# Performance work log

Hardware: AMD Instinct MI355X
Metric: run time of the kernel (lower is better)

## Reference

```python
import jax, jax.numpy as jnp
import numpy as np
from jax import lax

B, CIN, HW = 4, 3, 256      # batch, image channels, image size
HID = 128                   # hidden_size
EMB_D = 64                  # embedding_dim == encoder output channels
K = 1024                    # num_embeddings
L = 2                       # num encoder/decoder layers (1 resblock each)


def _conv(x, w, b, stride, pad):
    y = lax.conv_general_dilated(x, w, (stride, stride), ((pad, pad), (pad, pad)),
                                 dimension_numbers=('NCHW', 'OIHW', 'NCHW'))
    return y + b[None, :, None, None]


def _bn(x):
    # BatchNorm2d in training mode: batch stats over (N,H,W), affine at init (gamma=1, beta=0)
    m = x.mean((0, 2, 3), keepdims=True)
    v = x.var((0, 2, 3), keepdims=True)
    return (x - m) * lax.rsqrt(v + 1e-5)


def _resblock(x, w1, b1, w2, b2):
    y = jax.nn.relu(_bn(_conv(x, w1, b1, 1, 1)))
    y = _bn(_conv(y, w2, b2, 1, 1))
    return jax.nn.relu(y + x)


def _conv_t(x, w, b):
    # torch ConvTranspose2d(k=4, s=2, p=1); w in torch layout (I, O, 4, 4)
    wf = jnp.flip(w, (2, 3)).transpose(1, 0, 2, 3)  # (O, I, 4, 4)
    y = lax.conv_general_dilated(x, wf, (1, 1), ((2, 2), (2, 2)), lhs_dilation=(2, 2),
                                 dimension_numbers=('NCHW', 'OIHW', 'NCHW'))
    return y + b[None, :, None, None]


def _vqvae(x, enc_in_w, enc_in_b, enc_res_w1, enc_res_b1, enc_res_w2, enc_res_b2,
           enc_down_w, enc_down_b, enc_out_w, enc_out_b,
           dec_in_w, dec_in_b, dec_res_w1, dec_res_b1, dec_res_w2, dec_res_b2,
           dec_up_w, dec_up_b, dec_out_w, dec_out_b, codebook):
    sg = lax.stop_gradient
    # ---- encoder ----
    h = _conv(x, enc_in_w, enc_in_b, 1, 0)
    for i in range(L):
        h = _resblock(h, enc_res_w1[i], enc_res_b1[i], enc_res_w2[i], enc_res_b2[i])
        h = jax.nn.relu(_conv(h, enc_down_w[i], enc_down_b[i], 2, 1))
    z = _conv(h, enc_out_w, enc_out_b, 1, 0)  # (B, C, H/4, W/4)
    # ---- vector quantize ----
    Bz, C, Hl, Wl = z.shape
    zf = z.transpose(0, 2, 3, 1).reshape(-1, C)  # (N, C)
    # ||z - e||^2 expanded; same argmin as the (N,K,C) form without materializing it
    d = (zf * zf).sum(1, keepdims=True) - 2.0 * (zf @ codebook.T) + (codebook * codebook).sum(1)[None, :]
    idx = jnp.argmin(d, axis=1)  # (N,)
    z_q = codebook[idx].reshape(Bz, Hl, Wl, C).transpose(0, 3, 1, 2)
    z_q_st = z_q + sg(z - z_q)  # as in source: forward value == z, grads flow to codebook
    # ---- decoder ----
    h = _conv(z_q_st, dec_in_w, dec_in_b, 1, 0)
    for i in range(L):
        h = _resblock(h, dec_res_w1[i], dec_res_b1[i], dec_res_w2[i], dec_res_b2[i])
        h = jax.nn.relu(_conv_t(h, dec_up_w[i], dec_up_b[i]))
    recon = jax.nn.sigmoid(_conv(h, dec_out_w, dec_out_b, 1, 0))
    # ---- losses ----
    commit = jnp.mean((z - sg(z_q_st)) ** 2)
    cb_l = jnp.mean((sg(z) - z_q_st) ** 2)
    counts = jnp.zeros((K,), jnp.float32).at[idx].add(1.0)
    p = counts + 1e-6
    p = p / p.sum()
    ent = -(p * jnp.log(p)).sum()
    loss = commit + cb_l - ent
    return recon, loss, idx.reshape(Bz, Hl, Wl)


def setup_inputs() -> dict:
    key = jax.random.key(0)
    ks = iter(jax.random.split(key, 40))
    def w(shape, fan_in):
        return jax.random.normal(next(ks), shape, jnp.float32) * np.float32((2.0 / fan_in) ** 0.5)
    z128 = lambda *s: jnp.zeros(s, jnp.float32)
    return {
        'x': jax.random.uniform(next(ks), (B, CIN, HW, HW), jnp.float32),
        'enc_in_w': w((HID, CIN, 1, 1), CIN), 'enc_in_b': z128(HID),
        'enc_res_w1': w((L, HID, HID, 3, 3), HID * 9), 'enc_res_b1': z128(L, HID),
        'enc_res_w2': w((L, HID, HID, 3, 3), HID * 9), 'enc_res_b2': z128(L, HID),
        'enc_down_w': w((L, HID, HID, 4, 4), HID * 16), 'enc_down_b': z128(L, HID),
        'enc_out_w': w((EMB_D, HID, 1, 1), HID), 'enc_out_b': z128(EMB_D),
        'dec_in_w': w((HID, EMB_D, 1, 1), EMB_D), 'dec_in_b': z128(HID),
        'dec_res_w1': w((L, HID, HID, 3, 3), HID * 9), 'dec_res_b1': z128(L, HID),
        'dec_res_w2': w((L, HID, HID, 3, 3), HID * 9), 'dec_res_b2': z128(L, HID),
        'dec_up_w': w((L, HID, HID, 4, 4), HID * 16), 'dec_up_b': z128(L, HID),  # (I,O,4,4) torch layout
        'dec_out_w': w((CIN, HID, 1, 1), HID), 'dec_out_b': z128(CIN),
        'codebook': jax.random.normal(next(ks), (K, EMB_D), jnp.float32) * np.float32((2.0 / (K + EMB_D)) ** 0.5),
    }


def reference(x, enc_in_w, enc_in_b, enc_res_w1, enc_res_b1, enc_res_w2, enc_res_b2,
              enc_down_w, enc_down_b, enc_out_w, enc_out_b,
              dec_in_w, dec_in_b, dec_res_w1, dec_res_b1, dec_res_w2, dec_res_b2,
              dec_up_w, dec_up_b, dec_out_w, dec_out_b, codebook):
    return _vqvae(x, enc_in_w, enc_in_b, enc_res_w1, enc_res_b1, enc_res_w2, enc_res_b2,
                  enc_down_w, enc_down_b, enc_out_w, enc_out_b,
                  dec_in_w, dec_in_b, dec_res_w1, dec_res_b1, dec_res_w2, dec_res_b2,
                  dec_up_w, dec_up_b, dec_out_w, dec_out_b, codebook)
```

## Files before the change

kernel.cpp:

```cpp
#include <hip/hip_runtime.h>
#include <math.h>


#define RE_SIZE 786432

typedef float f32x4 __attribute__((ext_vector_type(4)));
typedef short bf16x8 __attribute__((ext_vector_type(8)));
typedef short bf16x4 __attribute__((ext_vector_type(4)));

__device__ __forceinline__ unsigned short f2bf(float f) {
  unsigned u = __float_as_uint(f);
  return (unsigned short)((u + 0x7fffu + ((u >> 16) & 1u)) >> 16);
}
__device__ __forceinline__ float bf2f(unsigned short h) {
  return __uint_as_float(((unsigned)h) << 16);
}
__device__ __forceinline__ void split3(float v, unsigned short& a,
                                       unsigned short& b, unsigned short& c) {
  a = f2bf(v); float r = v - bf2f(a);
  b = f2bf(r); r -= bf2f(b);
  c = f2bf(r);
}

__global__ __launch_bounds__(256) void weff_kernel(
    const float* __restrict__ w3, const float* __restrict__ ew,
    const float* __restrict__ eb, unsigned short* __restrict__ f0,
    unsigned short* __restrict__ f1, unsigned short* __restrict__ f2) {
  int id = blockIdx.x * 256 + threadIdx.x;
  int j = id & 7, lane = (id >> 3) & 63, mt = (id >> 9) & 7, kc = id >> 12;
  int co = mt * 16 + (lane & 15);
  int q = lane >> 4;
  int k = kc * 32 + q * 8 + j;
  int t = k >> 2, c = k & 3;
  float v = 0.f;
  if (t <= 8) {
    double acc = 0.0;
    for (int ci = 0; ci < 128; ++ci) {
      double wv = (double)w3[((long)co * 128 + ci) * 9 + t];
      double xv = (c < 3) ? (double)ew[ci * 3 + c] : (double)eb[ci];
      acc += wv * xv;
    }
    v = (float)acc;
  }
  unsigned short a, b, cc; split3(v, a, b, cc);
  f0[id] = a; f1[id] = b; f2[id] = cc;
}

__global__ __launch_bounds__(256) void conv36_mfma_kernel(
    const float* __restrict__ xin, const unsigned short* __restrict__ f0,
    const unsigned short* __restrict__ f1, const unsigned short* __restrict__ f2,
    const float* __restrict__ bias, float* __restrict__ out, int H, int W) {
  __shared__ __align__(16) unsigned short s_x[3][720];
  int tid = threadIdx.x, wv = tid >> 6, lane = tid & 63;
  int q = lane >> 4, c15 = lane & 15;
  int tilesX = W >> 4;
  int tx0 = (blockIdx.x % tilesX) << 4;
  int ty0 = (blockIdx.x / tilesX) << 3;
  int n = blockIdx.z;
  long HWl = (long)H * W;
  long ibase = (long)n * 128 * HWl;
  long xbase = (long)n * 3 * HWl;
  f32x4 acc[2][8];
#pragma unroll
  for (int a = 0; a < 2; ++a)
#pragma unroll
    for (int b = 0; b < 8; ++b) acc[a][b] = (f32x4){0.f, 0.f, 0.f, 0.f};

  for (int l = tid; l < 180; l += 256) {
    int y = l / 18, x = l % 18;
    int gy = ty0 + y - 1, gx = tx0 + x - 1;
    float v[4] = {0.f, 0.f, 0.f, 0.f};
    if ((unsigned)gy < (unsigned)H && (unsigned)gx < (unsigned)W) {
      const float* xp = xin + xbase + (long)gy * W + gx;
      v[0] = xp[0]; v[1] = xp[HWl]; v[2] = xp[2 * HWl]; v[3] = 1.f;
    }
    bf16x4 s0, s1, s2;
#pragma unroll
    for (int c = 0; c < 4; ++c) {
      unsigned short h0, h1, h2; split3(v[c], h0, h1, h2);
      s0[c] = (short)h0; s1[c] = (short)h1; s2[c] = (short)h2;
    }
    *(bf16x4*)(s_x[0] + l * 4) = s0;
    *(bf16x4*)(s_x[1] + l * 4) = s1;
    *(bf16x4*)(s_x[2] + l * 4) = s2;
  }
  __syncthreads();

#pragma unroll
  for (int kc = 0; kc < 2; ++kc) {
    bf16x8 a0[2], a1[2], a2[2];
#pragma unroll
    for (int m = 0; m < 2; ++m) {
      long fi = (long)(kc * 8 + 2 * wv + m) * 64 + lane;
      a0[m] = ((const bf16x8*)f0)[fi];
      a1[m] = ((const bf16x8*)f1)[fi];
      a2[m] = ((const bf16x8*)f2)[fi];
    }
    int ta = kc * 8 + 2 * q; if (ta > 8) ta = 8;
    int tb = ta + 1;         if (tb > 8) tb = 8;
    int pa_d = (ta / 3) * 18 + ta % 3;
    int pb_d = (tb / 3) * 18 + tb % 3;
#pragma unroll
    for (int nn = 0; nn < 8; ++nn) {
      int pa = (nn * 18 + c15 + pa_d) * 4;
      int pb = (nn * 18 + c15 + pb_d) * 4;
      bf16x8 b0, b1v, b2;
      bf16x4 lo, hi;
      lo = *(const bf16x4*)(s_x[0] + pa); hi = *(const bf16x4*)(s_x[0] + pb);
#pragma unroll
      for (int i = 0; i < 4; ++i) { b0[i] = lo[i]; b0[4 + i] = hi[i]; }
      lo = *(const bf16x4*)(s_x[1] + pa); hi = *(const bf16x4*)(s_x[1] + pb);
#pragma unroll
      for (int i = 0; i < 4; ++i) { b1v[i] = lo[i]; b1v[4 + i] = hi[i]; }
      lo = *(const bf16x4*)(s_x[2] + pa); hi = *(const bf16x4*)(s_x[2] + pb);
#pragma unroll
      for (int i = 0; i < 4; ++i) { b2[i] = lo[i]; b2[4 + i] = hi[i]; }
#pragma unroll
      for (int m = 0; m < 2; ++m) {
        acc[m][nn] = __builtin_amdgcn_mfma_f32_16x16x32_bf16(a0[m], b0, acc[m][nn], 0, 0, 0);
        acc[m][nn] = __builtin_amdgcn_mfma_f32_16x16x32_bf16(a0[m], b1v, acc[m][nn], 0, 0, 0);
        acc[m][nn] = __builtin_amdgcn_mfma_f32_16x16x32_bf16(a1[m], b0, acc[m][nn], 0, 0, 0);
        acc[m][nn] = __builtin_amdgcn_mfma_f32_16x16x32_bf16(a0[m], b2, acc[m][nn], 0, 0, 0);
        acc[m][nn] = __builtin_amdgcn_mfma_f32_16x16x32_bf16(a1[m], b1v, acc[m][nn], 0, 0, 0);
        acc[m][nn] = __builtin_amdgcn_mfma_f32_16x16x32_bf16(a2[m], b0, acc[m][nn], 0, 0, 0);
      }
    }
  }
#pragma unroll
  for (int mt2 = 0; mt2 < 2; ++mt2) {
    int co0 = (wv * 2 + mt2) * 16 + q * 4;
#pragma unroll
    for (int nn = 0; nn < 8; ++nn) {
      long pxoff = ibase + (long)(ty0 + nn) * W + tx0 + c15;
#pragma unroll
      for (int r = 0; r < 4; ++r)
        out[pxoff + (long)(co0 + r) * HWl] = acc[mt2][nn][r] + bias[co0 + r];
    }
  }
}

__global__ __launch_bounds__(256) void wsplit_kernel(
    const float* __restrict__ w, unsigned short* __restrict__ w0,
    unsigned short* __restrict__ w1, unsigned short* __restrict__ w2) {
  int id = blockIdx.x * 256 + threadIdx.x;
  int j = id & 7, lane = (id >> 3) & 63, rest = id >> 9;
  int mt = rest & 7, rest2 = rest >> 3;
  int tap = rest2 % 9, cc = rest2 / 9;
  int co = mt * 16 + (lane & 15);
  int ci = cc * 32 + (lane >> 4) * 8 + j;
  float v = w[((long)co * 128 + ci) * 9 + tap];
  unsigned short a, b, c; split3(v, a, b, c);
  w0[id] = a; w1[id] = b; w2[id] = c;
}

__global__ __launch_bounds__(256) void wsplit4_kernel(
    const float* __restrict__ w, unsigned short* __restrict__ w0,
    unsigned short* __restrict__ w1, unsigned short* __restrict__ w2) {
  int id = blockIdx.x * 256 + threadIdx.x;
  int j = id & 7, lane = (id >> 3) & 63;
  int mt = (id >> 9) & 7, pair = (id >> 12) & 7, cc = id >> 15;
  int q = lane >> 4;
  int tap = pair * 2 + (q >> 1);
  int ky = tap >> 2, kx = tap & 3;
  int co = mt * 16 + (lane & 15);
  int ci = cc * 16 + (q & 1) * 8 + j;
  float v = w[((long)co * 128 + ci) * 16 + ky * 4 + kx];
  unsigned short a, b, c; split3(v, a, b, c);
  w0[id] = a; w1[id] = b; w2[id] = c;
}

__global__ __launch_bounds__(256) void wsplitT_kernel(
    const float* __restrict__ w, unsigned short* __restrict__ w0,
    unsigned short* __restrict__ w1) {
  int id = blockIdx.x * 256 + threadIdx.x;
  int jj = id & 7, lane = (id >> 3) & 63;
  int mt = (id >> 9) & 7, j = (id >> 12) & 3, cls = (id >> 14) & 3, cc = id >> 16;
  int py = cls >> 1, px = cls & 1, jy = j >> 1, jx = j & 1;
  int ky = py ? (jy ? 2 : 0) : (jy ? 3 : 1);
  int kx = px ? (jx ? 2 : 0) : (jx ? 3 : 1);
  int co = mt * 16 + (lane & 15);
  int ci = cc * 32 + (lane >> 4) * 8 + jj;
  float v = w[((long)ci * 128 + co) * 16 + ky * 4 + kx];
  unsigned short h = f2bf(v);
  w0[id] = h;
  w1[id] = f2bf(v - bf2f(h));
}

template<int IMODE, int SPLIT>
__global__ __launch_bounds__(256) void conv3x3_mfma_kernel(
    const float* __restrict__ in, const unsigned short* __restrict__ w0s,
    const unsigned short* __restrict__ w1s, const unsigned short* __restrict__ w2s,
    const float* __restrict__ bias, float* __restrict__ out, int H, int W,
    const float2* __restrict__ mr, const float* __restrict__ xin,
    const float* __restrict__ w1, const float* __restrict__ b1) {
  __shared__ __align__(16) unsigned short s_x[SPLIT][5760];
  int tid = threadIdx.x, wv = tid >> 6, lane = tid & 63;
  int q = lane >> 4, c15 = lane & 15;
  int tilesX = W >> 4;
  int tx0 = (blockIdx.x % tilesX) << 4;
  int ty0 = (blockIdx.x / tilesX) << 3;
  int n = blockIdx.z;
  long HWl = (long)H * W;
  long ibase = (long)n * 128 * HWl;
  f32x4 acc[2][8];
#pragma unroll
  for (int a = 0; a < 2; ++a)
#pragma unroll
    for (int b = 0; b < 8; ++b) acc[a][b] = (f32x4){0.f, 0.f, 0.f, 0.f};

  for (int cc = 0; cc < 4; ++cc) {
    __syncthreads();
    for (int l = tid; l < 720; l += 256) {
      int cig = l / 180, px = l % 180;
      int y = px / 18, x = px % 18;
      int gy = ty0 + y - 1, gx = tx0 + x - 1;
      float v[8];
      if ((unsigned)gy < (unsigned)H && (unsigned)gx < (unsigned)W) {
        if (IMODE == 2) {
          const float* xp = xin + (long)n * 3 * HWl + (long)gy * W + gx;
          float x0 = xp[0], x1 = xp[HWl], x2 = xp[2 * HWl];
#pragma unroll
          for (int c = 0; c < 8; ++c) {
            int ci = cc * 32 + cig * 8 + c;
            v[c] = fmaf(w1[ci * 3 + 0], x0,
                   fmaf(w1[ci * 3 + 1], x1,
                   fmaf(w1[ci * 3 + 2], x2, b1[ci])));
          }
        } else {
          const float* ip = in + ibase + (long)(cc * 32 + cig * 8) * HWl
                            + (long)gy * W + gx;
#pragma unroll
          for (int c = 0; c < 8; ++c) v[c] = ip[(long)c * HWl];
          if (IMODE == 1) {
#pragma unroll
            for (int c = 0; c < 8; ++c) {
              float2 s = mr[cc * 32 + cig * 8 + c];
              v[c] = fmaxf((v[c] - s.x) * s.y, 0.f);
            }
          }
        }
      } else {
#pragma unroll
        for (int c = 0; c < 8; ++c) v[c] = 0.f;
      }
      bf16x8 sv[SPLIT];
#pragma unroll
      for (int c = 0; c < 8; ++c) {
        unsigned short h0 = f2bf(v[c]); float r = v[c] - bf2f(h0);
        unsigned short h1 = f2bf(r);
        sv[0][c] = (short)h0; sv[1][c] = (short)h1;
        if (SPLIT == 3) { r -= bf2f(h1); sv[2][c] = (short)f2bf(r); }
      }
#pragma unroll
      for (int s = 0; s < SPLIT; ++s) *(bf16x8*)(s_x[s] + l * 8) = sv[s];
    }
    __syncthreads();

    for (int tap = 0; tap < 9; ++tap) {
      int dy = tap / 3, dx = tap % 3;
      long fbase = (long)((cc * 9 + tap) * 8) * 64;
      bf16x8 a0[2], a1[2], a2[2];
#pragma unroll
      for (int m = 0; m < 2; ++m) {
        long fi = fbase + (2 * wv + m) * 64 + lane;
        a0[m] = ((const bf16x8*)w0s)[fi];
        a1[m] = ((const bf16x8*)w1s)[fi];
        if (SPLIT == 3) a2[m] = ((const bf16x8*)w2s)[fi];
      }
      int xoff = (q * 180 + dy * 18 + c15 + dx) * 8;
#pragma unroll
      for (int nn = 0; nn < 8; ++nn) {
        bf16x8 b0 = *(const bf16x8*)(s_x[0] + xoff + nn * 144);
        bf16x8 b1v = *(const bf16x8*)(s_x[1] + xoff + nn * 144);
#pragma unroll
        for (int m = 0; m < 2; ++m) {
          acc[m][nn] = __builtin_amdgcn_mfma_f32_16x16x32_bf16(a0[m], b0, acc[m][nn], 0, 0, 0);
          acc[m][nn] = __builtin_amdgcn_mfma_f32_16x16x32_bf16(a0[m], b1v, acc[m][nn], 0, 0, 0);
          acc[m][nn] = __builtin_amdgcn_mfma_f32_16x16x32_bf16(a1[m], b0, acc[m][nn], 0, 0, 0);
        }
        if (SPLIT == 3) {
          bf16x8 b2 = *(const bf16x8*)(s_x[2] + xoff + nn * 144);
#pragma unroll
          for (int m = 0; m < 2; ++m) {
            acc[m][nn] = __builtin_amdgcn_mfma_f32_16x16x32_bf16(a0[m], b2, acc[m][nn], 0, 0, 0);
            acc[m][nn] = __builtin_amdgcn_mfma_f32_16x16x32_bf16(a1[m], b1v, acc[m][nn], 0, 0, 0);
            acc[m][nn] = __builtin_amdgcn_mfma_f32_16x16x32_bf16(a2[m], b0, acc[m][nn], 0, 0, 0);
          }
        }
      }
    }
  }
#pragma unroll
  for (int mt2 = 0; mt2 < 2; ++mt2) {
    int co0 = (wv * 2 + mt2) * 16 + q * 4;
#pragma unroll
    for (int nn = 0; nn < 8; ++nn) {
      long pxoff = ibase + (long)(ty0 + nn) * W + tx0 + c15;
#pragma unroll
      for (int r = 0; r < 4; ++r)
        out[pxoff + (long)(co0 + r) * HWl] = acc[mt2][nn][r] + bias[co0 + r];
    }
  }
}

__global__ __launch_bounds__(256) void down_mfma_kernel(
    const float* __restrict__ in, const unsigned short* __restrict__ w0s,
    const unsigned short* __restrict__ w1s, const unsigned short* __restrict__ w2s,
    const float* __restrict__ bias, float* __restrict__ out, int Hin, int Win) {
  __shared__ __align__(16) unsigned short s_x[3][9792];
  int tid = threadIdx.x, wv = tid >> 6, lane = tid & 63;
  int q = lane >> 4, c15 = lane & 15;
  int Hout = Hin >> 1, Wout = Win >> 1;
  int tilesX = Wout >> 4;
  int tx0 = (blockIdx.x % tilesX) << 4;
  int ty0 = (blockIdx.x / tilesX) << 3;
  int n = blockIdx.z;
  long HWin = (long)Hin * Win, HWout = (long)Hout * Wout;
  long ibase = (long)n * 128 * HWin, obase = (long)n * 128 * HWout;
  f32x4 acc[2][8];
#pragma unroll
  for (int a = 0; a < 2; ++a)
#pragma unroll
    for (int b = 0; b < 8; ++b) acc[a][b] = (f32x4){0.f, 0.f, 0.f, 0.f};

  for (int cc = 0; cc < 8; ++cc) {
    __syncthreads();
    for (int l = tid; l < 1224; l += 256) {
      int cig = l / 612, rem = l % 612;
      int g = rem / 153, p = rem % 153;
      int py = p / 17, px_ = p % 17;
      int gy = g >> 1, gx = g & 1;
      int iy = 2 * (ty0 + py - gy) + gy;
      int ix = 2 * (tx0 + px_ - gx) + gx;
      float v[8];
      if ((unsigned)iy < (unsigned)Hin && (unsigned)ix < (unsigned)Win) {
        const float* ip = in + ibase + (long)(cc * 16 + cig * 8) * HWin
                          + (long)iy * Win + ix;
#pragma unroll
        for (int c = 0; c < 8; ++c) v[c] = ip[(long)c * HWin];
      } else {
#pragma unroll
        for (int c = 0; c < 8; ++c) v[c] = 0.f;
      }
      bf16x8 s0, s1, s2;
#pragma unroll
      for (int c = 0; c < 8; ++c) {
        unsigned short h0, h1, h2; split3(v[c], h0, h1, h2);
        s0[c] = (short)h0; s1[c] = (short)h1; s2[c] = (short)h2;
      }
      *(bf16x8*)(s_x[0] + l * 8) = s0;
      *(bf16x8*)(s_x[1] + l * 8) = s1;
      *(bf16x8*)(s_x[2] + l * 8) = s2;
    }
    __syncthreads();

    for (int pr = 0; pr < 8; ++pr) {
      long fbase = (long)((cc * 8 + pr) * 8) * 64;
      bf16x8 a0[2], a1[2], a2[2];
#pragma unroll
      for (int m = 0; m < 2; ++m) {
        long fi = fbase + (2 * wv + m) * 64 + lane;
        a0[m] = ((const bf16x8*)w0s)[fi];
        a1[m] = ((const bf16x8*)w1s)[fi];
        a2[m] = ((const bf16x8*)w2s)[fi];
      }
      int tap = pr * 2 + (q >> 1);
      int ky = tap >> 2, kx = tap & 3;
      int gy = (ky + 1) & 1, gx = (kx + 1) & 1;
      int dy = (ky == 0) ? -1 : ((ky == 3) ? 1 : 0);
      int dx = (kx == 0) ? -1 : ((kx == 3) ? 1 : 0);
      int g = gy * 2 + gx, cig = q & 1;
      int xoff = ((cig * 4 + g) * 153 + (dy + gy) * 17 + (c15 + dx + gx)) * 8;
#pragma unroll
      for (int nn = 0; nn < 8; ++nn) {
        bf16x8 b0 = *(const bf16x8*)(s_x[0] + xoff + nn * 136);
        bf16x8 b1v = *(const bf16x8*)(s_x[1] + xoff + nn * 136);
        bf16x8 b2 = *(const bf16x8*)(s_x[2] + xoff + nn * 136);
#pragma unroll
        for (int m = 0; m < 2; ++m) {
          acc[m][nn] = __builtin_amdgcn_mfma_f32_16x16x32_bf16(a0[m], b0, acc[m][nn], 0, 0, 0);
          acc[m][nn] = __builtin_amdgcn_mfma_f32_16x16x32_bf16(a0[m], b1v, acc[m][nn], 0, 0, 0);
          acc[m][nn] = __builtin_amdgcn_mfma_f32_16x16x32_bf16(a1[m], b0, acc[m][nn], 0, 0, 0);
          acc[m][nn] = __builtin_amdgcn_mfma_f32_16x16x32_bf16(a0[m], b2, acc[m][nn], 0, 0, 0);
          acc[m][nn] = __builtin_amdgcn_mfma_f32_16x16x32_bf16(a1[m], b1v, acc[m][nn], 0, 0, 0);
          acc[m][nn] = __builtin_amdgcn_mfma_f32_16x16x32_bf16(a2[m], b0, acc[m][nn], 0, 0, 0);
        }
      }
    }
  }
#pragma unroll
  for (int mt2 = 0; mt2 < 2; ++mt2) {
    int co0 = (wv * 2 + mt2) * 16 + q * 4;
#pragma unroll
    for (int nn = 0; nn < 8; ++nn) {
      long pxoff = obase + (long)(ty0 + nn) * Wout + tx0 + c15;
#pragma unroll
      for (int r = 0; r < 4; ++r)
        out[pxoff + (long)(co0 + r) * HWout] =
            fmaxf(acc[mt2][nn][r] + bias[co0 + r], 0.f);
    }
  }
}

__global__ __launch_bounds__(256) void up_mfma_kernel(
    const float* __restrict__ in, const unsigned short* __restrict__ wh,
    const unsigned short* __restrict__ wl, const float* __restrict__ bias,
    float* __restrict__ out, int Hin, int Win) {
  __shared__ __align__(16) unsigned short s_xh[5760];
  __shared__ __align__(16) unsigned short s_xl[5760];
  int tid = threadIdx.x, wv = tid >> 6, lane = tid & 63;
  int q = lane >> 4, c15 = lane & 15;
  int cls = blockIdx.z & 3, n = blockIdx.z >> 2;
  int py = cls >> 1, px = cls & 1;
  int Hout = Hin << 1, Wout = Win << 1;
  int tilesX = Win >> 4;
  int x0 = (blockIdx.x % tilesX) << 4;
  int m0 = (blockIdx.x / tilesX) << 3;
  long HWin = (long)Hin * Win, HWout = (long)Hout * Wout;
  long ibase = (long)n * 128 * HWin, obase = (long)n * 128 * HWout;
  f32x4 acc[2][8];
#pragma unroll
  for (int a = 0; a < 2; ++a)
#pragma unroll
    for (int b = 0; b < 8; ++b) acc[a][b] = (f32x4){0.f, 0.f, 0.f, 0.f};

  for (int cc = 0; cc < 4; ++cc) {
    __syncthreads();
    for (int l = tid; l < 720; l += 256) {
      int cig = l / 180, p = l % 180;
      int y = p / 18, x = p % 18;
      int gy = m0 + y - 1, gx = x0 + x - 1;
      float v[8];
      if ((unsigned)gy < (unsigned)Hin && (unsigned)gx < (unsigned)Win) {
        const float* ip = in + ibase + (long)(cc * 32 + cig * 8) * HWin
                          + (long)gy * Win + gx;
#pragma unroll
        for (int c = 0; c < 8; ++c) v[c] = ip[(long)c * HWin];
      } else {
#pragma unroll
        for (int c = 0; c < 8; ++c) v[c] = 0.f;
      }
      bf16x8 hv, lv;
#pragma unroll
      for (int c = 0; c < 8; ++c) {
        unsigned short h = f2bf(v[c]);
        hv[c] = (short)h;
        lv[c] = (short)f2bf(v[c] - bf2f(h));
      }
      *(bf16x8*)(s_xh + l * 8) = hv;
      *(bf16x8*)(s_xl + l * 8) = lv;
    }
    __syncthreads();

#pragma unroll
    for (int j = 0; j < 4; ++j) {
      int jy = j >> 1, jx = j & 1;
      int dy = py ? (jy ? 0 : 1) : (jy ? -1 : 0);
      int dx = px ? (jx ? 0 : 1) : (jx ? -1 : 0);
      long fbase = (long)((((cc * 4 + cls) * 4 + j) * 8)) * 64;
      const bf16x8* aph = (const bf16x8*)wh + fbase;
      const bf16x8* apl = (const bf16x8*)wl + fbase;
      bf16x8 ah0 = aph[(2 * wv) * 64 + lane];
      bf16x8 ah1 = aph[(2 * wv + 1) * 64 + lane];
      bf16x8 al0 = apl[(2 * wv) * 64 + lane];
      bf16x8 al1 = apl[(2 * wv + 1) * 64 + lane];
      int xoff = (q * 180 + (dy + 1) * 18 + (c15 + dx + 1)) * 8;
#pragma unroll
      for (int nn = 0; nn < 8; ++nn) {
        bf16x8 bh = *(const bf16x8*)(s_xh + xoff + nn * 144);
        bf16x8 bl = *(const bf16x8*)(s_xl + xoff + nn * 144);
        acc[0][nn] = __builtin_amdgcn_mfma_f32_16x16x32_bf16(ah0, bh, acc[0][nn], 0, 0, 0);
        acc[0][nn] = __builtin_amdgcn_mfma_f32_16x16x32_bf16(ah0, bl, acc[0][nn], 0, 0, 0);
        acc[0][nn] = __builtin_amdgcn_mfma_f32_16x16x32_bf16(al0, bh, acc[0][nn], 0, 0, 0);
        acc[1][nn] = __builtin_amdgcn_mfma_f32_16x16x32_bf16(ah1, bh, acc[1][nn], 0, 0, 0);
        acc[1][nn] = __builtin_amdgcn_mfma_f32_16x16x32_bf16(ah1, bl, acc[1][nn], 0, 0, 0);
        acc[1][nn] = __builtin_amdgcn_mfma_f32_16x16x32_bf16(al1, bh, acc[1][nn], 0, 0, 0);
      }
    }
  }
#pragma unroll
  for (int mt2 = 0; mt2 < 2; ++mt2) {
    int co0 = (wv * 2 + mt2) * 16 + q * 4;
#pragma unroll
    for (int nn = 0; nn < 8; ++nn) {
      long pxoff = obase + (long)(2 * (m0 + nn) + py) * Wout + 2 * (x0 + c15) + px;
#pragma unroll
      for (int r = 0; r < 4; ++r)
        out[pxoff + (long)(co0 + r) * HWout] =
            fmaxf(acc[mt2][nn][r] + bias[co0 + r], 0.f);
    }
  }
}

template<int ACT, int CW>
__global__ __launch_bounds__(256) void conv1x1_kernel(
    const float* __restrict__ in, const float* __restrict__ w,
    const float* __restrict__ bias, float* __restrict__ out,
    int N, int Cin, int Cout, int HW) {
  extern __shared__ float wl[];
  int co0 = blockIdx.y * CW;
  for (int i = threadIdx.x; i < CW * Cin; i += blockDim.x)
    wl[i] = w[(long)co0 * Cin + i];
  __syncthreads();
  int HW4 = HW >> 2;
  long p4 = (long)blockIdx.x * blockDim.x + threadIdx.x;
  if (p4 >= (long)N * HW4) return;
  int n = (int)(p4 / HW4), hw4 = (int)(p4 % HW4);
  const float4* inp = (const float4*)(in + (long)n * Cin * HW) + hw4;
  float4* outp = (float4*)(out + (long)n * Cout * HW) + hw4;
  float4 acc[CW];
#pragma unroll
  for (int j = 0; j < CW; ++j) { float bb = bias[co0 + j]; acc[j] = make_float4(bb, bb, bb, bb); }
  for (int ci = 0; ci < Cin; ++ci) {
    float4 v = inp[(long)ci * HW4];
#pragma unroll
    for (int j = 0; j < CW; ++j) {
      float ww = wl[j * Cin + ci];
      acc[j].x = fmaf(ww, v.x, acc[j].x);
      acc[j].y = fmaf(ww, v.y, acc[j].y);
      acc[j].z = fmaf(ww, v.z, acc[j].z);
      acc[j].w = fmaf(ww, v.w, acc[j].w);
    }
  }
#pragma unroll
  for (int j = 0; j < CW; ++j) {
    float4 v = acc[j];
    if (ACT == 2) {
      v.x = 1.f / (1.f + expf(-v.x));
      v.y = 1.f / (1.f + expf(-v.y));
      v.z = 1.f / (1.f + expf(-v.z));
      v.w = 1.f / (1.f + expf(-v.w));
    }
    outp[(long)(co0 + j) * HW4] = v;
  }
}

__global__ __launch_bounds__(256) void bn_part_kernel(
    const float* __restrict__ x, float2* __restrict__ part, int HW) {
  int c = blockIdx.x, sl = blockIdx.y, tid = threadIdx.x;
  int seg = HW >> 3;
  double s = 0.0, ss = 0.0;
  for (int n = 0; n < 4; ++n) {
    const float4* xp = (const float4*)(x + ((long)(n * 128 + c)) * HW + (long)sl * seg);
    for (int i = tid; i < (seg >> 2); i += 256) {
      float4 v = xp[i];
      s  += (double)v.x + (double)v.y + (double)v.z + (double)v.w;
      ss += (double)v.x * v.x + (double)v.y * v.y + (double)v.z * v.z + (double)v.w * v.w;
    }
  }
  __shared__ double shs[256], shss[256];
  shs[tid] = s; shss[tid] = ss;
  __syncthreads();
  for (int off = 128; off > 0; off >>= 1) {
    if (tid < off) { shs[tid] += shs[tid + off]; shss[tid] += shss[tid + off]; }
    __syncthreads();
  }
  if (tid == 0) part[c * 8 + sl] = make_float2((float)shs[0], (float)shss[0]);
}

__global__ __launch_bounds__(128) void bn_final_kernel(
    const float2* __restrict__ part, float2* __restrict__ mr, float cntf) {
  int c = threadIdx.x;
  if (c < 128) {
    double s = 0.0, ss = 0.0;
#pragma unroll
    for (int i = 0; i < 8; ++i) { float2 p = part[c * 8 + i]; s += p.x; ss += p.y; }
    double cnt = (double)cntf;
    double m = s / cnt;
    double var = ss / cnt - m * m;
    mr[c] = make_float2((float)m, (float)(1.0 / sqrt(var + 1e-5)));
  }
}

template<int RMODE>
__global__ __launch_bounds__(256) void bn_res_relu_kernel(
    float* __restrict__ y, const float2* __restrict__ mr,
    const float* __restrict__ res,
    const float* __restrict__ xin, const float* __restrict__ w1,
    const float* __restrict__ b1, int HW4) {
  int nc = blockIdx.y;
  int c = nc & 127, n = nc >> 7;
  float2 s = mr[c];
  int i = blockIdx.x * blockDim.x + threadIdx.x;
  if (i >= HW4) return;
  long off = (long)nc * HW4 + i;
  float4 v = ((const float4*)y)[off];
  v.x = (v.x - s.x) * s.y; v.y = (v.y - s.x) * s.y;
  v.z = (v.z - s.x) * s.y; v.w = (v.w - s.x) * s.y;
  float4 r4;
  if (RMODE == 0) {
    r4 = ((const float4*)res)[off];
  } else {
    const float4* xp = (const float4*)(xin) + (long)n * 3 * HW4 + i;
    float4 x0 = xp[0], x1 = xp[HW4], x2 = xp[2 * HW4];
    float wa = w1[c * 3 + 0], wb = w1[c * 3 + 1], wc = w1[c * 3 + 2], bb = b1[c];
    r4.x = fmaf(wa, x0.x, fmaf(wb, x1.x, fmaf(wc, x2.x, bb)));
    r4.y = fmaf(wa, x0.y, fmaf(wb, x1.y, fmaf(wc, x2.y, bb)));
    r4.z = fmaf(wa, x0.z, fmaf(wb, x1.z, fmaf(wc, x2.z, bb)));
    r4.w = fmaf(wa, x0.w, fmaf(wb, x1.w, fmaf(wc, x2.w, bb)));
  }
  v.x = fmaxf(v.x + r4.x, 0.f); v.y = fmaxf(v.y + r4.y, 0.f);
  v.z = fmaxf(v.z + r4.z, 0.f); v.w = fmaxf(v.w + r4.w, 0.f);
  ((float4*)y)[off] = v;
}

__global__ __launch_bounds__(256) void vq_kernel(
    const float* __restrict__ z, const float* __restrict__ cb,
    float* __restrict__ idx_out, float* __restrict__ counts, int HWl) {
  __shared__ float s_z[64][65];
  __shared__ float s_cb[64][64];
  __shared__ float s_bd[4][64];
  __shared__ int   s_bk[4][64];
  int tid = threadIdx.x;
  int r0 = blockIdx.x * 64;
  for (int l = tid; l < 64 * 64; l += 256) {
    int c = l >> 6, rs = l & 63;
    int r = r0 + rs;
    int n = r / HWl, rem = r % HWl;
    s_z[rs][c] = z[((long)(n * 64 + c)) * HWl + rem];
  }
  int row = tid & 63, cg = tid >> 6;
  float best = 3.4e38f; int bestk = 0;
  for (int k0 = 0; k0 < 1024; k0 += 64) {
    __syncthreads();
    for (int l = tid; l < 4096; l += 256)
      s_cb[l >> 6][l & 63] = cb[(long)(k0 + (l >> 6)) * 64 + (l & 63)];
    __syncthreads();
#pragma unroll
    for (int j = 0; j < 16; ++j) {
      int kk = cg * 16 + j;
      const float* zp = s_z[row];
      const float* cp = s_cb[kk];
      float d = 0.f;
#pragma unroll
      for (int c = 0; c < 64; ++c) {
        float t = zp[c] - cp[c];
        d = fmaf(t, t, d);
      }
      int k = k0 + kk;
      if (d < best) { best = d; bestk = k; }
    }
  }
  s_bd[cg][row] = best; s_bk[cg][row] = bestk;
  __syncthreads();
  if (tid < 64) {
    float bd = s_bd[0][tid]; int bk = s_bk[0][tid];
#pragma unroll
    for (int g = 1; g < 4; ++g) {
      float d2 = s_bd[g][tid]; int k2 = s_bk[g][tid];
      if (d2 < bd || (d2 == bd && k2 < bk)) { bd = d2; bk = k2; }
    }
    idx_out[r0 + tid] = (float)bk;
    atomicAdd(&counts[bk], 1.0f);
  }
}

__global__ __launch_bounds__(256) void zero_kernel(float* __restrict__ p, int n) {
  int i = blockIdx.x * 256 + threadIdx.x;
  if (i < n) p[i] = 0.f;
}

__global__ __launch_bounds__(256) void entropy_kernel(
    const float* __restrict__ counts, float* __restrict__ loss_out) {
  __shared__ double sh[256];
  int tid = threadIdx.x;
  double s = 0.0;
  for (int i = tid; i < 1024; i += 256) s += (double)counts[i] + 1e-6;
  sh[tid] = s; __syncthreads();
  for (int off = 128; off > 0; off >>= 1) {
    if (tid < off) sh[tid] += sh[tid + off];
    __syncthreads();
  }
  double S = sh[0];
  __syncthreads();
  double pl = 0.0;
  for (int i = tid; i < 1024; i += 256) {
    double p = ((double)counts[i] + 1e-6) / S;
    pl += p * log(p);
  }
  sh[tid] = pl; __syncthreads();
  for (int off = 128; off > 0; off >>= 1) {
    if (tid < off) sh[tid] += sh[tid + off];
    __syncthreads();
  }
  if (tid == 0) loss_out[0] = (float)sh[0];
}

extern "C" void kernel_launch(void* const* d_in, const int* in_sizes, int n_in,
                              void* d_out, int out_size, void* d_ws, size_t ws_size,
                              hipStream_t stream) {
  (void)in_sizes; (void)n_in; (void)out_size; (void)ws_size;
  const float* x          = (const float*)d_in[0];
  const float* enc_in_w   = (const float*)d_in[1];
  const float* enc_in_b   = (const float*)d_in[2];
  const float* enc_res_w1 = (const float*)d_in[3];
  const float* enc_res_b1 = (const float*)d_in[4];
  const float* enc_res_w2 = (const float*)d_in[5];
  const float* enc_res_b2 = (const float*)d_in[6];
  const float* enc_down_w = (const float*)d_in[7];
  const float* enc_down_b = (const float*)d_in[8];
  const float* enc_out_w  = (const float*)d_in[9];
  const float* enc_out_b  = (const float*)d_in[10];
  const float* dec_in_w   = (const float*)d_in[11];
  const float* dec_in_b   = (const float*)d_in[12];
  const float* dec_res_w1 = (const float*)d_in[13];
  const float* dec_res_b1 = (const float*)d_in[14];
  const float* dec_res_w2 = (const float*)d_in[15];
  const float* dec_res_b2 = (const float*)d_in[16];
  const float* dec_up_w   = (const float*)d_in[17];
  const float* dec_up_b   = (const float*)d_in[18];
  const float* dec_out_w  = (const float*)d_in[19];
  const float* dec_out_b  = (const float*)d_in[20];
  const float* codebook   = (const float*)d_in[21];
  float* out = (float*)d_out;

  const long BIG = 33554432;
  const long S1 = 8388608, S2 = 16777216, S3 = 25165824;
  float* P0 = (float*)d_ws;
  float* P1 = P0 + BIG;
  float2* mr   = (float2*)out;
  float* hist  = out + 256;
  float2* part = (float2*)(out + 1280);
  unsigned short* W0 = (unsigned short*)(out + 4096);
  unsigned short* W1 = (unsigned short*)(out + 135168);
  unsigned short* W2 = (unsigned short*)(out + 266240);
  unsigned short* F0 = (unsigned short*)(out + 401408);
  unsigned short* F1 = F0 + 8192;
  unsigned short* F2 = F1 + 8192;

  const int W3 = 128 * 128 * 9, W4 = 128 * 128 * 16, BS = 128;
  const dim3 g256(512, 1, 4), g128(128, 1, 4), g64(32, 1, 4);

  weff_kernel<<<32, 256, 0, stream>>>(enc_res_w1, enc_in_w, enc_in_b, F0, F1, F2);
  conv36_mfma_kernel<<<g256, 256, 0, stream>>>(
      x, F0, F1, F2, enc_res_b1, P0, 256, 256);
  bn_part_kernel<<<dim3(128, 8), 256, 0, stream>>>(P0, part, 65536);
  bn_final_kernel<<<1, 128, 0, stream>>>(part, mr, 262144.f);
  wsplit_kernel<<<576, 256, 0, stream>>>(enc_res_w2, W0, W1, W2);
  conv3x3_mfma_kernel<1, 3><<<g256, 256, 0, stream>>>(
      P0, W0, W1, W2, enc_res_b2, P1, 256, 256, mr, nullptr, nullptr, nullptr);
  bn_part_kernel<<<dim3(128, 8), 256, 0, stream>>>(P1, part, 65536);
  bn_final_kernel<<<1, 128, 0, stream>>>(part, mr, 262144.f);
  bn_res_relu_kernel<1><<<dim3(64, 512), 256, 0, stream>>>(
      P1, mr, nullptr, x, enc_in_w, enc_in_b, 16384);
  wsplit4_kernel<<<1024, 256, 0, stream>>>(enc_down_w, W0, W1, W2);
  down_mfma_kernel<<<g128, 256, 0, stream>>>(P1, W0, W1, W2, enc_down_b, P0, 256, 256);

  wsplit_kernel<<<576, 256, 0, stream>>>(enc_res_w1 + W3, W0, W1, W2);
  conv3x3_mfma_kernel<0, 3><<<g128, 256, 0, stream>>>(
      P0, W0, W1, W2, enc_res_b1 + BS, P0 + S1, 128, 128, nullptr, nullptr, nullptr, nullptr);
  bn_part_kernel<<<dim3(128, 8), 256, 0, stream>>>(P0 + S1, part, 16384);
  bn_final_kernel<<<1, 128, 0, stream>>>(part, mr, 65536.f);
  wsplit_kernel<<<576, 256, 0, stream>>>(enc_res_w2 + W3, W0, W1, W2);
  conv3x3_mfma_kernel<1, 3><<<g128, 256, 0, stream>>>(
      P0 + S1, W0, W1, W2, enc_res_b2 + BS, P0 + S2, 128, 128, mr, nullptr, nullptr, nullptr);
  bn_part_kernel<<<dim3(128, 8), 256, 0, stream>>>(P0 + S2, part, 16384);
  bn_final_kernel<<<1, 128, 0, stream>>>(part, mr, 65536.f);
  bn_res_relu_kernel<0><<<dim3(16, 512), 256, 0, stream>>>(
      P0 + S2, mr, P0, nullptr, nullptr, nullptr, 4096);
  wsplit4_kernel<<<1024, 256, 0, stream>>>(enc_down_w + W4, W0, W1, W2);
  down_mfma_kernel<<<g64, 256, 0, stream>>>(P0 + S2, W0, W1, W2, enc_down_b + BS, P0 + S3, 128, 128);

  conv1x1_kernel<0, 16><<<dim3(16, 4), 256, 16 * 128 * 4, stream>>>(
      P0 + S3, enc_out_w, enc_out_b, P1, 4, 128, 64, 4096);

  zero_kernel<<<4, 256, 0, stream>>>(hist, 1024);
  vq_kernel<<<256, 256, 0, stream>>>(P1, codebook, out + RE_SIZE + 1, hist, 4096);
  entropy_kernel<<<1, 256, 0, stream>>>(hist, out + RE_SIZE);

  conv1x1_kernel<0, 16><<<dim3(16, 8), 256, 16 * 64 * 4, stream>>>(
      P1, dec_in_w, dec_in_b, P0, 4, 64, 128, 4096);

  wsplit_kernel<<<576, 256, 0, stream>>>(dec_res_w1, W0, W1, W2);
  conv3x3_mfma_kernel<0, 2><<<g64, 256, 0, stream>>>(
      P0, W0, W1, W2, dec_res_b1, P0 + S1, 64, 64, nullptr, nullptr, nullptr, nullptr);
  bn_part_kernel<<<dim3(128, 8), 256, 0, stream>>>(P0 + S1, part, 4096);
  bn_final_kernel<<<1, 128, 0, stream>>>(part, mr, 16384.f);
  wsplit_kernel<<<576, 256, 0, stream>>>(dec_res_w2, W0, W1, W2);
  conv3x3_mfma_kernel<1, 2><<<g64, 256, 0, stream>>>(
      P0 + S1, W0, W1, W2, dec_res_b2, P0 + S2, 64, 64, mr, nullptr, nullptr, nullptr);
  bn_part_kernel<<<dim3(128, 8), 256, 0, stream>>>(P0 + S2, part, 4096);
  bn_final_kernel<<<1, 128, 0, stream>>>(part, mr, 16384.f);
  bn_res_relu_kernel<0><<<dim3(4, 512), 256, 0, stream>>>(
      P0 + S2, mr, P0, nullptr, nullptr, nullptr, 1024);
  wsplitT_kernel<<<1024, 256, 0, stream>>>(dec_up_w, W0, W1);
  up_mfma_kernel<<<dim3(32, 1, 16), 256, 0, stream>>>(
      P0 + S2, W0, W1, dec_up_b, P0 + S3, 64, 64);

  wsplit_kernel<<<576, 256, 0, stream>>>(dec_res_w1 + W3, W0, W1, W2);
  conv3x3_mfma_kernel<0, 2><<<g128, 256, 0, stream>>>(
      P0 + S3, W0, W1, W2, dec_res_b1 + BS, P1, 128, 128, nullptr, nullptr, nullptr, nullptr);
  bn_part_kernel<<<dim3(128, 8), 256, 0, stream>>>(P1, part, 16384);
  bn_final_kernel<<<1, 128, 0, stream>>>(part, mr, 65536.f);
  wsplit_kernel<<<576, 256, 0, stream>>>(dec_res_w2 + W3, W0, W1, W2);
  conv3x3_mfma_kernel<1, 2><<<g128, 256, 0, stream>>>(
      P1, W0, W1, W2, dec_res_b2 + BS, P1 + S1, 128, 128, mr, nullptr, nullptr, nullptr);
  bn_part_kernel<<<dim3(128, 8), 256, 0, stream>>>(P1 + S1, part, 16384);
  bn_final_kernel<<<1, 128, 0, stream>>>(part, mr, 65536.f);
  bn_res_relu_kernel<0><<<dim3(16, 512), 256, 0, stream>>>(
      P1 + S1, mr, P0 + S3, nullptr, nullptr, nullptr, 4096);
  wsplitT_kernel<<<1024, 256, 0, stream>>>(dec_up_w + W4, W0, W1);
  up_mfma_kernel<<<dim3(128, 1, 16), 256, 0, stream>>>(
      P1 + S1, W0, W1, dec_up_b + BS, P0, 128, 128);

  conv1x1_kernel<2, 3><<<dim3(256, 1), 256, 3 * 128 * 4, stream>>>(
      P0, dec_out_w, dec_out_b, out, 4, 128, 3, 65536);
}
```

Measured before the change: 1.651 ms.

## Fuse BN+residual+ReLU into down/up conv input staging; rework VQ kernel

Three of the four resblock-ending BN+residual+ReLU passes are folded into the following downsample or transposed-conv kernels, which now normalize, add the residual and apply ReLU while loading input tiles. In the first encoder stage the residual (the 1x1 input conv of the image) is recomputed on the fly. This removes full-tensor read/write passes and kernel launches. The halo pixels are recomputed in overlapping tiles, and the residual read is added to the conv loaders. Separately, the VQ kernel keeps each row's z in registers and loads the codebook with float4 in a different k ordering.

```diff
diff --git a/kernel.cpp b/kernel.cpp
--- a/kernel.cpp
+++ b/kernel.cpp
@@ -191,8 +191,7 @@
     const float* __restrict__ in, const unsigned short* __restrict__ w0s,
     const unsigned short* __restrict__ w1s, const unsigned short* __restrict__ w2s,
     const float* __restrict__ bias, float* __restrict__ out, int H, int W,
-    const float2* __restrict__ mr, const float* __restrict__ xin,
-    const float* __restrict__ w1, const float* __restrict__ b1) {
+    const float2* __restrict__ mr) {
   __shared__ __align__(16) unsigned short s_x[SPLIT][5760];
   int tid = threadIdx.x, wv = tid >> 6, lane = tid & 63;
   int q = lane >> 4, c15 = lane & 15;
@@ -216,27 +215,15 @@
       int gy = ty0 + y - 1, gx = tx0 + x - 1;
       float v[8];
       if ((unsigned)gy < (unsigned)H && (unsigned)gx < (unsigned)W) {
-        if (IMODE == 2) {
-          const float* xp = xin + (long)n * 3 * HWl + (long)gy * W + gx;
-          float x0 = xp[0], x1 = xp[HWl], x2 = xp[2 * HWl];
+        const float* ip = in + ibase + (long)(cc * 32 + cig * 8) * HWl
+                          + (long)gy * W + gx;
+#pragma unroll
+        for (int c = 0; c < 8; ++c) v[c] = ip[(long)c * HWl];
+        if (IMODE == 1) {
 #pragma unroll
           for (int c = 0; c < 8; ++c) {
-            int ci = cc * 32 + cig * 8 + c;
-            v[c] = fmaf(w1[ci * 3 + 0], x0,
-                   fmaf(w1[ci * 3 + 1], x1,
-                   fmaf(w1[ci * 3 + 2], x2, b1[ci])));
-          }
-        } else {
-          const float* ip = in + ibase + (long)(cc * 32 + cig * 8) * HWl
-                            + (long)gy * W + gx;
-#pragma unroll
-          for (int c = 0; c < 8; ++c) v[c] = ip[(long)c * HWl];
-          if (IMODE == 1) {
-#pragma unroll
-            for (int c = 0; c < 8; ++c) {
-              float2 s = mr[cc * 32 + cig * 8 + c];
-              v[c] = fmaxf((v[c] - s.x) * s.y, 0.f);
-            }
+            float2 s = mr[cc * 32 + cig * 8 + c];
+            v[c] = fmaxf((v[c] - s.x) * s.y, 0.f);
           }
         }
       } else {
@@ -303,10 +290,14 @@
   }
 }
 
+template<int IMODE>
 __global__ __launch_bounds__(256) void down_mfma_kernel(
     const float* __restrict__ in, const unsigned short* __restrict__ w0s,
     const unsigned short* __restrict__ w1s, const unsigned short* __restrict__ w2s,
-    const float* __restrict__ bias, float* __restrict__ out, int Hin, int Win) {
+    const float* __restrict__ bias, float* __restrict__ out, int Hin, int Win,
+    const float2* __restrict__ mr, const float* __restrict__ res,
+    const float* __restrict__ xin, const float* __restrict__ ew,
+    const float* __restrict__ eb) {
   __shared__ __align__(16) unsigned short s_x[3][9792];
   int tid = threadIdx.x, wv = tid >> 6, lane = tid & 63;
   int q = lane >> 4, c15 = lane & 15;
@@ -334,10 +325,29 @@
       int ix = 2 * (tx0 + px_ - gx) + gx;
       float v[8];
       if ((unsigned)iy < (unsigned)Hin && (unsigned)ix < (unsigned)Win) {
-        const float* ip = in + ibase + (long)(cc * 16 + cig * 8) * HWin
-                          + (long)iy * Win + ix;
+        int cb0 = cc * 16 + cig * 8;
+        const float* ip = in + ibase + (long)cb0 * HWin + (long)iy * Win + ix;
 #pragma unroll
         for (int c = 0; c < 8; ++c) v[c] = ip[(long)c * HWin];
+        float x0 = 0.f, x1 = 0.f, x2 = 0.f;
+        if (IMODE == 2) {
+          const float* xp = xin + (long)n * 3 * HWin + (long)iy * Win + ix;
+          x0 = xp[0]; x1 = xp[HWin]; x2 = xp[2 * HWin];
+        }
+        const float* rp = (IMODE == 1)
+            ? res + ibase + (long)cb0 * HWin + (long)iy * Win + ix : nullptr;
+#pragma unroll
+        for (int c = 0; c < 8; ++c) {
+          float2 s = mr[cb0 + c];
+          float rv;
+          if (IMODE == 1) rv = rp[(long)c * HWin];
+          else {
+            int ci = cb0 + c;
+            rv = fmaf(ew[ci * 3 + 0], x0, fmaf(ew[ci * 3 + 1], x1,
+                 fmaf(ew[ci * 3 + 2], x2, eb[ci])));
+          }
+          v[c] = fmaxf((v[c] - s.x) * s.y + rv, 0.f);
+        }
       } else {
 #pragma unroll
         for (int c = 0; c < 8; ++c) v[c] = 0.f;
@@ -402,10 +412,12 @@
   }
 }
 
+template<int UMODE>
 __global__ __launch_bounds__(256) void up_mfma_kernel(
     const float* __restrict__ in, const unsigned short* __restrict__ wh,
     const unsigned short* __restrict__ wl, const float* __restrict__ bias,
-    float* __restrict__ out, int Hin, int Win) {
+    float* __restrict__ out, int Hin, int Win,
+    const float2* __restrict__ mr, const float* __restrict__ res) {
   __shared__ __align__(16) unsigned short s_xh[5760];
   __shared__ __align__(16) unsigned short s_xl[5760];
   int tid = threadIdx.x, wv = tid >> 6, lane = tid & 63;
@@ -432,10 +444,18 @@
       int gy = m0 + y - 1, gx = x0 + x - 1;
       float v[8];
       if ((unsigned)gy < (unsigned)Hin && (unsigned)gx < (unsigned)Win) {
-        const float* ip = in + ibase + (long)(cc * 32 + cig * 8) * HWin
-                          + (long)gy * Win + gx;
+        int cb0 = cc * 32 + cig * 8;
+        const float* ip = in + ibase + (long)cb0 * HWin + (long)gy * Win + gx;
 #pragma unroll
         for (int c = 0; c < 8; ++c) v[c] = ip[(long)c * HWin];
+        if (UMODE == 1) {
+          const float* rp = res + ibase + (long)cb0 * HWin + (long)gy * Win + gx;
+#pragma unroll
+          for (int c = 0; c < 8; ++c) {
+            float2 s = mr[cb0 + c];
+            v[c] = fmaxf((v[c] - s.x) * s.y + rp[(long)c * HWin], 0.f);
+          }
+        }
       } else {
 #pragma unroll
         for (int c = 0; c < 8; ++c) v[c] = 0.f;
@@ -572,85 +592,73 @@
   }
 }
 
-template<int RMODE>
 __global__ __launch_bounds__(256) void bn_res_relu_kernel(
     float* __restrict__ y, const float2* __restrict__ mr,
-    const float* __restrict__ res,
-    const float* __restrict__ xin, const float* __restrict__ w1,
-    const float* __restrict__ b1, int HW4) {
+    const float* __restrict__ res, int HW4) {
   int nc = blockIdx.y;
-  int c = nc & 127, n = nc >> 7;
+  int c = nc & 127;
   float2 s = mr[c];
   int i = blockIdx.x * blockDim.x + threadIdx.x;
   if (i >= HW4) return;
   long off = (long)nc * HW4 + i;
   float4 v = ((const float4*)y)[off];
-  v.x = (v.x - s.x) * s.y; v.y = (v.y - s.x) * s.y;
-  v.z = (v.z - s.x) * s.y; v.w = (v.w - s.x) * s.y;
-  float4 r4;
-  if (RMODE == 0) {
-    r4 = ((const float4*)res)[off];
-  } else {
-    const float4* xp = (const float4*)(xin) + (long)n * 3 * HW4 + i;
-    float4 x0 = xp[0], x1 = xp[HW4], x2 = xp[2 * HW4];
-    float wa = w1[c * 3 + 0], wb = w1[c * 3 + 1], wc = w1[c * 3 + 2], bb = b1[c];
-    r4.x = fmaf(wa, x0.x, fmaf(wb, x1.x, fmaf(wc, x2.x, bb)));
-    r4.y = fmaf(wa, x0.y, fmaf(wb, x1.y, fmaf(wc, x2.y, bb)));
-    r4.z = fmaf(wa, x0.z, fmaf(wb, x1.z, fmaf(wc, x2.z, bb)));
-    r4.w = fmaf(wa, x0.w, fmaf(wb, x1.w, fmaf(wc, x2.w, bb)));
-  }
-  v.x = fmaxf(v.x + r4.x, 0.f); v.y = fmaxf(v.y + r4.y, 0.f);
-  v.z = fmaxf(v.z + r4.z, 0.f); v.w = fmaxf(v.w + r4.w, 0.f);
+  float4 r4 = ((const float4*)res)[off];
+  v.x = fmaxf((v.x - s.x) * s.y + r4.x, 0.f);
+  v.y = fmaxf((v.y - s.x) * s.y + r4.y, 0.f);
+  v.z = fmaxf((v.z - s.x) * s.y + r4.z, 0.f);
+  v.w = fmaxf((v.w - s.x) * s.y + r4.w, 0.f);
   ((float4*)y)[off] = v;
 }
 
 __global__ __launch_bounds__(256) void vq_kernel(
     const float* __restrict__ z, const float* __restrict__ cb,
     float* __restrict__ idx_out, float* __restrict__ counts, int HWl) {
-  __shared__ float s_z[64][65];
-  __shared__ float s_cb[64][64];
+  __shared__ __align__(16) float s_cb[4096];
   __shared__ float s_bd[4][64];
   __shared__ int   s_bk[4][64];
   int tid = threadIdx.x;
-  int r0 = blockIdx.x * 64;
-  for (int l = tid; l < 64 * 64; l += 256) {
-    int c = l >> 6, rs = l & 63;
-    int r = r0 + rs;
-    int n = r / HWl, rem = r % HWl;
-    s_z[rs][c] = z[((long)(n * 64 + c)) * HWl + rem];
-  }
-  int row = tid & 63, cg = tid >> 6;
+  int rs = tid & 63, g = tid >> 6;
+  int r = blockIdx.x * 64 + rs;
+  int n = r / HWl, rem = r % HWl;
+  float zr[64];
+#pragma unroll
+  for (int c = 0; c < 64; ++c) zr[c] = z[((long)(n * 64 + c)) * HWl + rem];
   float best = 3.4e38f; int bestk = 0;
-  for (int k0 = 0; k0 < 1024; k0 += 64) {
-    __syncthreads();
-    for (int l = tid; l < 4096; l += 256)
-      s_cb[l >> 6][l & 63] = cb[(long)(k0 + (l >> 6)) * 64 + (l & 63)];
-    __syncthreads();
-#pragma unroll
+  for (int it = 0; it < 16; ++it) {
+    __syncthreads();
+    for (int l = tid; l < 1024; l += 256) {
+      int s = l >> 4, c4 = (l & 15) << 2;
+      int k = (s >> 4) * 256 + it * 16 + (s & 15);
+      *(float4*)(s_cb + s * 64 + c4) = *(const float4*)(cb + (long)k * 64 + c4);
+    }
+    __syncthreads();
+#pragma unroll 4
     for (int j = 0; j < 16; ++j) {
-      int kk = cg * 16 + j;
-      const float* zp = s_z[row];
-      const float* cp = s_cb[kk];
+      const float* cp = s_cb + (g * 16 + j) * 64;
       float d = 0.f;
 #pragma unroll
-      for (int c = 0; c < 64; ++c) {
-        float t = zp[c] - cp[c];
-        d = fmaf(t, t, d);
-      }
-      int k = k0 + kk;
+      for (int cq = 0; cq < 16; ++cq) {
+        float4 cv = *(const float4*)(cp + cq * 4);
+        float t;
+        t = zr[cq * 4 + 0] - cv.x; d = fmaf(t, t, d);
+        t = zr[cq * 4 + 1] - cv.y; d = fmaf(t, t, d);
+        t = zr[cq * 4 + 2] - cv.z; d = fmaf(t, t, d);
+        t = zr[cq * 4 + 3] - cv.w; d = fmaf(t, t, d);
+      }
+      int k = g * 256 + it * 16 + j;
       if (d < best) { best = d; bestk = k; }
     }
   }
-  s_bd[cg][row] = best; s_bk[cg][row] = bestk;
+  s_bd[g][rs] = best; s_bk[g][rs] = bestk;
   __syncthreads();
   if (tid < 64) {
     float bd = s_bd[0][tid]; int bk = s_bk[0][tid];
 #pragma unroll
-    for (int g = 1; g < 4; ++g) {
-      float d2 = s_bd[g][tid]; int k2 = s_bk[g][tid];
+    for (int gg = 1; gg < 4; ++gg) {
+      float d2 = s_bd[gg][tid]; int k2 = s_bk[gg][tid];
       if (d2 < bd || (d2 == bd && k2 < bk)) { bd = d2; bk = k2; }
     }
-    idx_out[r0 + tid] = (float)bk;
+    idx_out[blockIdx.x * 64 + tid] = (float)bk;
     atomicAdd(&counts[bk], 1.0f);
   }
 }
@@ -738,28 +746,27 @@
   bn_final_kernel<<<1, 128, 0, stream>>>(part, mr, 262144.f);
   wsplit_kernel<<<576, 256, 0, stream>>>(enc_res_w2, W0, W1, W2);
   conv3x3_mfma_kernel<1, 3><<<g256, 256, 0, stream>>>(
-      P0, W0, W1, W2, enc_res_b2, P1, 256, 256, mr, nullptr, nullptr, nullptr);
+      P0, W0, W1, W2, enc_res_b2, P1, 256, 256, mr);
   bn_part_kernel<<<dim3(128, 8), 256, 0, stream>>>(P1, part, 65536);
   bn_final_kernel<<<1, 128, 0, stream>>>(part, mr, 262144.f);
-  bn_res_relu_kernel<1><<<dim3(64, 512), 256, 0, stream>>>(
-      P1, mr, nullptr, x, enc_in_w, enc_in_b, 16384);
   wsplit4_kernel<<<1024, 256, 0, stream>>>(enc_down_w, W0, W1, W2);
-  down_mfma_kernel<<<g128, 256, 0, stream>>>(P1, W0, W1, W2, enc_down_b, P0, 256, 256);
+  down_mfma_kernel<2><<<g128, 256, 0, stream>>>(
+      P1, W0, W1, W2, enc_down_b, P0, 256, 256, mr, nullptr, x, enc_in_w, enc_in_b);
 
   wsplit_kernel<<<576, 256, 0, stream>>>(enc_res_w1 + W3, W0, W1, W2);
   conv3x3_mfma_kernel<0, 3><<<g128, 256, 0, stream>>>(
-      P0, W0, W1, W2, enc_res_b1 + BS, P0 + S1, 128, 128, nullptr, nullptr, nullptr, nullptr);
+      P0, W0, W1, W2, enc_res_b1 + BS, P0 + S1, 128, 128, nullptr);
   bn_part_kernel<<<dim3(128, 8), 256, 0, stream>>>(P0 + S1, part, 16384);
   bn_final_kernel<<<1, 128, 0, stream>>>(part, mr, 65536.f);
   wsplit_kernel<<<576, 256, 0, stream>>>(enc_res_w2 + W3, W0, W1, W2);
   conv3x3_mfma_kernel<1, 3><<<g128, 256, 0, stream>>>(
-      P0 + S1, W0, W1, W2, enc_res_b2 + BS, P0 + S2, 128, 128, mr, nullptr, nullptr, nullptr);
+      P0 + S1, W0, W1, W2, enc_res_b2 + BS, P0 + S2, 128, 128, mr);
   bn_part_kernel<<<dim3(128, 8), 256, 0, stream>>>(P0 + S2, part, 16384);
   bn_final_kernel<<<1, 128, 0, stream>>>(part, mr, 65536.f);
-  bn_res_relu_kernel<0><<<dim3(16, 512), 256, 0, stream>>>(
-      P0 + S2, mr, P0, nullptr, nullptr, nullptr, 4096);
   wsplit4_kernel<<<1024, 256, 0, stream>>>(enc_down_w + W4, W0, W1, W2);
-  down_mfma_kernel<<<g64, 256, 0, stream>>>(P0 + S2, W0, W1, W2, enc_down_b + BS, P0 + S3, 128, 128);
+  down_mfma_kernel<1><<<g64, 256, 0, stream>>>(
+      P0 + S2, W0, W1, W2, enc_down_b + BS, P0 + S3, 128, 128, mr, P0,
+      nullptr, nullptr, nullptr);
 
   conv1x1_kernel<0, 16><<<dim3(16, 4), 256, 16 * 128 * 4, stream>>>(
       P0 + S3, enc_out_w, enc_out_b, P1, 4, 128, 64, 4096);
@@ -773,35 +780,33 @@
 
   wsplit_kernel<<<576, 256, 0, stream>>>(dec_res_w1, W0, W1, W2);
   conv3x3_mfma_kernel<0, 2><<<g64, 256, 0, stream>>>(
-      P0, W0, W1, W2, dec_res_b1, P0 + S1, 64, 64, nullptr, nullptr, nullptr, nullptr);
+      P0, W0, W1, W2, dec_res_b1, P0 + S1, 64, 64, nullptr);
   bn_part_kernel<<<dim3(128, 8), 256, 0, stream>>>(P0 + S1, part, 4096);
   bn_final_kernel<<<1, 128, 0, stream>>>(part, mr, 16384.f);
   wsplit_kernel<<<576, 256, 0, stream>>>(dec_res_w2, W0, W1, W2);
   conv3x3_mfma_kernel<1, 2><<<g64, 256, 0, stream>>>(
-      P0 + S1, W0, W1, W2, dec_res_b2, P0 + S2, 64, 64, mr, nullptr, nullptr, nullptr);
+      P0 + S1, W0, W1, W2, dec_res_b2, P0 + S2, 64, 64, mr);
   bn_part_kernel<<<dim3(128, 8), 256, 0, stream>>>(P0 + S2, part, 4096);
   bn_final_kernel<<<1, 128, 0, stream>>>(part, mr, 16384.f);
-  bn_res_relu_kernel<0><<<dim3(4, 512), 256, 0, stream>>>(
-      P0 + S2, mr, P0, nullptr, nullptr, nullptr, 1024);
   wsplitT_kernel<<<1024, 256, 0, stream>>>(dec_up_w, W0, W1);
-  up_mfma_kernel<<<dim3(32, 1, 16), 256, 0, stream>>>(
-      P0 + S2, W0, W1, dec_up_b, P0 + S3, 64, 64);
+  up_mfma_kernel<1><<<dim3(32, 1, 16), 256, 0, stream>>>(
+      P0 + S2, W0, W1, dec_up_b, P0 + S3, 64, 64, mr, P0);
 
   wsplit_kernel<<<576, 256, 0, stream>>>(dec_res_w1 + W3, W0, W1, W2);
   conv3x3_mfma_kernel<0, 2><<<g128, 256, 0, stream>>>(
-      P0 + S3, W0, W1, W2, dec_res_b1 + BS, P1, 128, 128, nullptr, nullptr, nullptr, nullptr);
+      P0 + S3, W0, W1, W2, dec_res_b1 + BS, P1, 128, 128, nullptr);
   bn_part_kernel<<<dim3(128, 8), 256, 0, stream>>>(P1, part, 16384);
   bn_final_kernel<<<1, 128, 0, stream>>>(part, mr, 65536.f);
   wsplit_kernel<<<576, 256, 0, stream>>>(dec_res_w2 + W3, W0, W1, W2);
   conv3x3_mfma_kernel<1, 2><<<g128, 256, 0, stream>>>(
-      P1, W0, W1, W2, dec_res_b2 + BS, P1 + S1, 128, 128, mr, nullptr, nullptr, nullptr);
+      P1, W0, W1, W2, dec_res_b2 + BS, P1 + S1, 128, 128, mr);
   bn_part_kernel<<<dim3(128, 8), 256, 0, stream>>>(P1 + S1, part, 16384);
   bn_final_kernel<<<1, 128, 0, stream>>>(part, mr, 65536.f);
-  bn_res_relu_kernel<0><<<dim3(16, 512), 256, 0, stream>>>(
-      P1 + S1, mr, P0 + S3, nullptr, nullptr, nullptr, 4096);
+  bn_res_relu_kernel<<<dim3(16, 512), 256, 0, stream>>>(
+      P1 + S1, mr, P0 + S3, 4096);
   wsplitT_kernel<<<1024, 256, 0, stream>>>(dec_up_w + W4, W0, W1);
-  up_mfma_kernel<<<dim3(128, 1, 16), 256, 0, stream>>>(
-      P1 + S1, W0, W1, dec_up_b + BS, P0, 128, 128);
+  up_mfma_kernel<0><<<dim3(128, 1, 16), 256, 0, stream>>>(
+      P1 + S1, W0, W1, dec_up_b + BS, P0, 128, 128, nullptr, nullptr);
 
   conv1x1_kernel<2, 3><<<dim3(256, 1), 256, 3 * 128 * 4, stream>>>(
       P0, dec_out_w, dec_out_b, out, 4, 128, 3, 65536);
```

Result: slower. 1.696 ms (+2.8%).
